# Optimization experiments

Hardware: AMD Instinct MI355X
Metric: run time of the kernel (lower is better)

## Reference

```python
import jax, jax.numpy as jnp
import numpy as np

B, N, C_IN, C_OUT, K = 8, 2048, 64, 128, 20
EPS = 1e-5  # BatchNorm2d default eps


def setup_inputs() -> dict:
    key = jax.random.key(0)
    k1, k2 = jax.random.split(key, 2)
    x = jax.random.normal(k1, (B, C_IN, N), dtype=jnp.float32)
    fan_in = 2 * C_IN
    W = jax.random.normal(k2, (C_OUT, 2 * C_IN), dtype=jnp.float32) / np.sqrt(fan_in).astype(np.float32)
    b = jnp.zeros((C_OUT,), jnp.float32)
    gamma = jnp.ones((C_OUT,), jnp.float32)
    beta = jnp.zeros((C_OUT,), jnp.float32)
    return {"x": x, "W": W, "b": b, "gamma": gamma, "beta": beta}


def reference(x, W, b, gamma, beta):
    # x: (B, C_in, N) -> points (B, N, C_in)
    pts = jnp.transpose(x, (0, 2, 1))
    # pairwise squared L2 distances (B, N, N)
    sq = jnp.sum(pts * pts, axis=-1)
    dist = sq[:, :, None] + sq[:, None, :] - 2.0 * jnp.einsum('bnc,bmc->bnm', pts, pts)
    # knn: top-k of negated distance -> k nearest neighbors (includes self)
    _, nn_idx = jax.lax.top_k(-dist, K)  # (B, N, K)
    # gather neighbor features per batch: (B, N, K, C_in)
    neigh = jax.vmap(lambda p, i: p[i])(pts, nn_idx)
    central = pts[:, :, None, :]  # (B, N, 1, C_in)
    edge = jnp.concatenate(
        [jnp.broadcast_to(central, neigh.shape), neigh - central], axis=-1
    )  # (B, N, K, 2*C_in)
    # 1x1 conv == channelwise linear: (B, N, K, C_out)
    y = jnp.einsum('bnkc,oc->bnko', edge, W) + b
    # BatchNorm2d (training mode): stats over batch + spatial dims, biased var
    mean = jnp.mean(y, axis=(0, 1, 2))
    var = jnp.var(y, axis=(0, 1, 2))
    y = (y - mean) * jax.lax.rsqrt(var + EPS) * gamma + beta
    y = jax.nn.relu(y)
    y = jnp.max(y, axis=2)  # max over k neighbors -> (B, N, C_out)
    return jnp.transpose(y, (0, 2, 1))[..., None]  # (B, C_out, N, 1)
```

## Files before the change

### kernel.cpp

```cpp
#include <hip/hip_runtime.h>
#include <cstdint>
#include <cstddef>

#define NPTS 2048
#define BATCH 8
#define CIN 64
#define CO 128
#define KNN 20
#define KSEL 24
#define NSPLIT 4
#define MKP 25

typedef short s16x8 __attribute__((ext_vector_type(8)));
typedef unsigned short u16x8 __attribute__((ext_vector_type(8)));
typedef float f32x4 __attribute__((ext_vector_type(4)));

__device__ inline unsigned short f2bf_rne(float x) {
  unsigned u = __float_as_uint(x);
  unsigned r = (u + 0x7FFFu + ((u >> 16) & 1u)) >> 16;
  return (unsigned short)r;
}
__device__ inline float bf2f(unsigned short h) {
  return __uint_as_float(((unsigned)h) << 16);
}
__device__ inline unsigned med3u(unsigned a, unsigned b, unsigned c) {
  unsigned d;
  asm("v_med3_u32 %0, %1, %2, %3" : "=v"(d) : "v"(a), "v"(b), "v"(c));
  return d;
}

__global__ __launch_bounds__(256) void prep_kernel(
    const float* __restrict__ x, float* __restrict__ P,
    unsigned short* __restrict__ PG, float* __restrict__ SQ,
    float* __restrict__ STATS) {
  __shared__ float tile[64 * 65];
  const int b = blockIdx.y, T = blockIdx.x, n0 = T * 64, tid = threadIdx.x;
  if (b == 0 && T == 0) {
    for (int t = tid; t < 5 * CO; t += 256) STATS[t] = 0.f;
  }
  const float* xb = x + (size_t)b * CIN * NPTS;
#pragma unroll
  for (int j = 0; j < 16; ++j) {
    int e = j * 256 + tid;
    int c = e >> 6, nl = e & 63;
    tile[c * 65 + nl] = xb[(size_t)c * NPTS + n0 + nl];
  }
  __syncthreads();
  float* Pb = P + (size_t)b * NPTS * CIN;
#pragma unroll
  for (int j = 0; j < 16; ++j) {
    int e = j * 256 + tid;
    int nl = e >> 6, c = e & 63;
    Pb[(size_t)(n0 + nl) * CIN + c] = tile[c * 65 + nl];
  }
  if (tid < 64) {
    float acc = 0.f;
#pragma unroll
    for (int c = 0; c < 64; ++c) {
      float v = tile[c * 65 + tid];
      acc = fmaf(v, v, acc);
    }
    SQ[(size_t)b * NPTS + n0 + tid] = acc;
  }
  const size_t tbase = (size_t)(b * 32 + T) * 8192;
#pragma unroll
  for (int j = 0; j < 2; ++j) {
    int c2 = j * 256 + tid;
    int row = c2 >> 3, kc = c2 & 7;
    int frag = ((row >> 4) << 1) | (kc >> 2);
    int lidx = (row & 15) | ((kc & 3) << 4);
    s16x8 hi8, lo8;
#pragma unroll
    for (int e = 0; e < 8; ++e) {
      float v = tile[(kc * 8 + e) * 65 + row];
      unsigned short hb = f2bf_rne(v);
      float hf = bf2f(hb);
      unsigned short lb = f2bf_rne(v - hf);
      hi8[e] = (short)hb;
      lo8[e] = (short)lb;
    }
    size_t co = (size_t)(frag * 64 + lidx) * 8;
    *(s16x8*)(PG + tbase + co) = hi8;
    *(s16x8*)(PG + tbase + 4096 + co) = lo8;
  }
}

__global__ __launch_bounds__(256) void knn_part_kernel(
    const unsigned short* __restrict__ PG, const float* __restrict__ SQ,
    unsigned* __restrict__ POOLS) {
  const int b = blockIdx.z;
  const int cs = blockIdx.y;
  const int n0 = blockIdx.x * 64;
  const int tid = threadIdx.x;
  const int lane = tid & 63, w = tid >> 6;
  const int qi = w * 16 + (lane & 15);
  const int sub = lane >> 4;
  const int T0 = cs * 8;

  __shared__ unsigned mk[64 * 4 * MKP];

  const size_t tqb = (size_t)(b * 32 + (n0 >> 6)) * 8192;
  const s16x8 qhi0 = *(const s16x8*)(PG + tqb + (size_t)((w * 2 + 0) * 64 + lane) * 8);
  const s16x8 qhi1 = *(const s16x8*)(PG + tqb + (size_t)((w * 2 + 1) * 64 + lane) * 8);
  const s16x8 qlo0 = *(const s16x8*)(PG + tqb + 4096 + (size_t)((w * 2 + 0) * 64 + lane) * 8);
  const s16x8 qlo1 = *(const s16x8*)(PG + tqb + 4096 + (size_t)((w * 2 + 1) * 64 + lane) * 8);

  unsigned hk[KSEL];
#pragma unroll
  for (int s = 0; s < KSEL; ++s) hk[s] = 0xFFFFFFFFu;

#pragma unroll 1
  for (int t = 0; t < 8; ++t) {
    const int T = T0 + t;
    const unsigned short* tb = PG + (size_t)(b * 32 + T) * 8192;
#pragma unroll
    for (int rt = 0; rt < 4; ++rt) {
      const s16x8 ahi0 = *(const s16x8*)(tb + (size_t)((rt * 2 + 0) * 64 + lane) * 8);
      const s16x8 ahi1 = *(const s16x8*)(tb + (size_t)((rt * 2 + 1) * 64 + lane) * 8);
      const s16x8 alo0 = *(const s16x8*)(tb + 4096 + (size_t)((rt * 2 + 0) * 64 + lane) * 8);
      const s16x8 alo1 = *(const s16x8*)(tb + 4096 + (size_t)((rt * 2 + 1) * 64 + lane) * 8);
      f32x4 acc = {0.f, 0.f, 0.f, 0.f};
      acc = __builtin_amdgcn_mfma_f32_16x16x32_bf16(alo0, qhi0, acc, 0, 0, 0);
      acc = __builtin_amdgcn_mfma_f32_16x16x32_bf16(ahi0, qlo0, acc, 0, 0, 0);
      acc = __builtin_amdgcn_mfma_f32_16x16x32_bf16(ahi0, qhi0, acc, 0, 0, 0);
      acc = __builtin_amdgcn_mfma_f32_16x16x32_bf16(alo1, qhi1, acc, 0, 0, 0);
      acc = __builtin_amdgcn_mfma_f32_16x16x32_bf16(ahi1, qlo1, acc, 0, 0, 0);
      acc = __builtin_amdgcn_mfma_f32_16x16x32_bf16(ahi1, qhi1, acc, 0, 0, 0);
      const float4 sq4 = *(const float4*)(SQ + b * NPTS + T * 64 + rt * 16 + sub * 4);
      const float sqa[4] = {sq4.x, sq4.y, sq4.z, sq4.w};
      const int mbase = T * 64 + rt * 16 + sub * 4;
#pragma unroll
      for (int r = 0; r < 4; ++r) {
        float d = fmaf(acc[r], -2.0f, sqa[r]);
        unsigned u = __float_as_uint(d);
        unsigned ord = u ^ (unsigned)(((int)u >> 31) | 0x80000000);
        unsigned key = (ord & 0xFFFFF800u) | (unsigned)(mbase + r);
#pragma unroll
        for (int s = KSEL - 1; s >= 1; --s) hk[s] = med3u(hk[s - 1], hk[s], key);
        hk[0] = hk[0] < key ? hk[0] : key;
      }
    }
  }

#pragma unroll
  for (int s = 0; s < KSEL; ++s) mk[(qi * 4 + sub) * MKP + s] = hk[s];
  __syncthreads();

  if (sub == 0) {
    const unsigned* bl = mk + qi * 4 * MKP;
    unsigned* pq = POOLS + ((size_t)(b * NPTS + n0 + qi) * NSPLIT + cs) * KSEL;
    int p0 = 0, p1 = 0, p2 = 0, p3 = 0;
#pragma unroll 1
    for (int s = 0; s < KSEL; ++s) {
      unsigned k0 = (p0 < KSEL) ? bl[0 * MKP + p0] : 0xFFFFFFFFu;
      unsigned k1 = (p1 < KSEL) ? bl[1 * MKP + p1] : 0xFFFFFFFFu;
      unsigned k2 = (p2 < KSEL) ? bl[2 * MKP + p2] : 0xFFFFFFFFu;
      unsigned k3 = (p3 < KSEL) ? bl[3 * MKP + p3] : 0xFFFFFFFFu;
      unsigned bk = k0; int bs = 0;
      if (k1 < bk) { bk = k1; bs = 1; }
      if (k2 < bk) { bk = k2; bs = 2; }
      if (k3 < bk) { bk = k3; bs = 3; }
      pq[s] = bk;
      if (bs == 0) ++p0; else if (bs == 1) ++p1; else if (bs == 2) ++p2; else ++p3;
    }
  }
}

__global__ __launch_bounds__(256) void knn_merge_kernel(
    const float* __restrict__ P, const unsigned* __restrict__ POOLS,
    int* __restrict__ IDX) {
  const int tid = threadIdx.x;
  const int qi = tid >> 3, st = tid & 7;
  const int r0 = blockIdx.x * 32;
  const int r = r0 + qi;
  const int b = r >> 11;

  __shared__ unsigned lists[32][NSPLIT][KSEL];
  __shared__ unsigned pool[32][KSEL];
  __shared__ double cd[32][KSEL];

  {
    const unsigned* src = POOLS + (size_t)r0 * NSPLIT * KSEL;
    for (int t = tid; t < 32 * NSPLIT * KSEL; t += 256) ((unsigned*)lists)[t] = src[t];
  }
  __syncthreads();

  if (st == 0) {
    const unsigned* bl = &lists[qi][0][0];
    unsigned* pq = &pool[qi][0];
    int p0 = 0, p1 = 0, p2 = 0, p3 = 0;
#pragma unroll 1
    for (int s = 0; s < KSEL; ++s) {
      unsigned k0 = (p0 < KSEL) ? bl[0 * KSEL + p0] : 0xFFFFFFFFu;
      unsigned k1 = (p1 < KSEL) ? bl[1 * KSEL + p1] : 0xFFFFFFFFu;
      unsigned k2 = (p2 < KSEL) ? bl[2 * KSEL + p2] : 0xFFFFFFFFu;
      unsigned k3 = (p3 < KSEL) ? bl[3 * KSEL + p3] : 0xFFFFFFFFu;
      unsigned bk = k0; int bs = 0;
      if (k1 < bk) { bk = k1; bs = 1; }
      if (k2 < bk) { bk = k2; bs = 2; }
      if (k3 < bk) { bk = k3; bs = 3; }
      pq[s] = bk;
      if (bs == 0) ++p0; else if (bs == 1) ++p1; else if (bs == 2) ++p2; else ++p3;
    }
  }
  __syncthreads();

  const float* qrow = P + ((size_t)r << 6);
  float4 q4[16];
#pragma unroll
  for (int t = 0; t < 16; ++t) q4[t] = ((const float4*)qrow)[t];
#pragma unroll 1
  for (int j = 0; j < 3; ++j) {
    int cand = st * 3 + j;
    unsigned key = pool[qi][cand];
    int m = (int)(key & 0x7FFu);
    const float* prow = P + ((size_t)(b * NPTS + m) << 6);
    double a0 = 0.0, a1 = 0.0;
#pragma unroll
    for (int t = 0; t < 16; ++t) {
      float4 pv = ((const float4*)prow)[t];
      double d0 = (double)pv.x - (double)q4[t].x;
      double d1 = (double)pv.y - (double)q4[t].y;
      double d2 = (double)pv.z - (double)q4[t].z;
      double d3 = (double)pv.w - (double)q4[t].w;
      a0 = fma(d1, d1, fma(d0, d0, a0));
      a1 = fma(d3, d3, fma(d2, d2, a1));
    }
    cd[qi][cand] = a0 + a1;
  }
  __syncthreads();

  int* op = IDX + (size_t)r * KNN;
#pragma unroll 1
  for (int j = 0; j < 3; ++j) {
    int cand = st * 3 + j;
    double dv = cd[qi][cand];
    int iv = (int)(pool[qi][cand] & 0x7FFu);
    int rk = 0;
#pragma unroll 1
    for (int t = 0; t < KSEL; ++t) {
      double dt = cd[qi][t];
      int it = (int)(pool[qi][t] & 0x7FFu);
      rk += ((dt < dv) || (dt == dv && it < iv)) ? 1 : 0;
    }
    if (rk < KNN) op[rk] = iv;
  }
}

__global__ __launch_bounds__(256) void proj_kernel(
    const float* __restrict__ P, const float* __restrict__ W,
    float* __restrict__ U, unsigned short* __restrict__ Vh) {
  const int r0 = blockIdx.x * 64;
  const int o0 = blockIdx.y * 32;
  const int tid = threadIdx.x;
  const int og = tid & 3;
  const int nl = tid >> 2;

  __shared__ float Pt[64 * 65];
  __shared__ float Wu_s[64 * 36];
  __shared__ float Wd_s[64 * 36];

#pragma unroll
  for (int j = 0; j < 16; ++j) {
    int e = j * 256 + tid;
    int c = e & 63, rl = e >> 6;
    Pt[rl * 65 + c] = P[((size_t)(r0 + rl) << 6) + c];
  }
#pragma unroll
  for (int j = 0; j < 8; ++j) {
    int e = j * 256 + tid;
    int c = e & 63, ol = e >> 6;
    float w1 = W[(size_t)(o0 + ol) * 128 + c];
    float w2 = W[(size_t)(o0 + ol) * 128 + 64 + c];
    Wu_s[c * 36 + ol] = w1 - w2;
    Wd_s[c * 36 + ol] = w2;
  }
  __syncthreads();

  float au[8] = {0,0,0,0,0,0,0,0};
  float av[8] = {0,0,0,0,0,0,0,0};
#pragma unroll 4
  for (int c = 0; c < 64; ++c) {
    float p = Pt[nl * 65 + c];
    const float* wu = Wu_s + c * 36 + og * 8;
    const float* wd = Wd_s + c * 36 + og * 8;
    float4 u0 = *(const float4*)wu;
    float4 u1 = *(const float4*)(wu + 4);
    float4 dd0 = *(const float4*)wd;
    float4 dd1 = *(const float4*)(wd + 4);
    au[0] = fmaf(p, u0.x, au[0]); au[1] = fmaf(p, u0.y, au[1]);
    au[2] = fmaf(p, u0.z, au[2]); au[3] = fmaf(p, u0.w, au[3]);
    au[4] = fmaf(p, u1.x, au[4]); au[5] = fmaf(p, u1.y, au[5]);
    au[6] = fmaf(p, u1.z, au[6]); au[7] = fmaf(p, u1.w, au[7]);
    av[0] = fmaf(p, dd0.x, av[0]); av[1] = fmaf(p, dd0.y, av[1]);
    av[2] = fmaf(p, dd0.z, av[2]); av[3] = fmaf(p, dd0.w, av[3]);
    av[4] = fmaf(p, dd1.x, av[4]); av[5] = fmaf(p, dd1.y, av[5]);
    av[6] = fmaf(p, dd1.z, av[6]); av[7] = fmaf(p, dd1.w, av[7]);
  }
  size_t ob = (size_t)(r0 + nl) * CO + o0 + og * 8;
  float4 s0 = {au[0], au[1], au[2], au[3]};
  float4 s1 = {au[4], au[5], au[6], au[7]};
  *(float4*)(U + ob) = s0;
  *(float4*)(U + ob + 4) = s1;
  u16x8 hv;
#pragma unroll
  for (int j = 0; j < 8; ++j) hv[j] = f2bf_rne(av[j]);
  *(u16x8*)(Vh + ob) = hv;
}

__global__ __launch_bounds__(256) void gstats_kernel(
    const float* __restrict__ U, const unsigned short* __restrict__ Vh,
    const int* __restrict__ IDX, float* __restrict__ Z, float* __restrict__ STATS) {
  const int r0 = blockIdx.x * 16;
  const int tid = threadIdx.x;
  const int og = tid & 15, nl = tid >> 4;
  const int r = r0 + nl;
  const int b = r >> 11;
  const unsigned short* Vb = Vh + ((size_t)b << 11) * CO;

  __shared__ int ii[16 * KNN];
  __shared__ float red[4][5][128];

  for (int t = tid; t < 16 * KNN; t += 256) ii[t] = IDX[(size_t)r0 * KNN + t];
  __syncthreads();

  float vmax[8], svr[8], svvr[8];
#pragma unroll
  for (int j = 0; j < 8; ++j) { vmax[j] = -3.4e38f; svr[j] = 0.f; svvr[j] = 0.f; }
#pragma unroll 1
  for (int k = 0; k < KNN; ++k) {
    int idx = ii[nl * KNN + k];
    u16x8 hv = *(const u16x8*)(Vb + (size_t)idx * CO + og * 8);
#pragma unroll
    for (int j = 0; j < 8; ++j) {
      float v = bf2f((unsigned short)hv[j]);
      vmax[j] = fmaxf(vmax[j], v);
      svr[j] += v;
      svvr[j] = fmaf(v, v, svvr[j]);
    }
  }
  size_t ob = (size_t)r * CO + og * 8;
  float4 u0 = *(const float4*)(U + ob);
  float4 u1 = *(const float4*)(U + ob + 4);
  float uu[8] = {u0.x, u0.y, u0.z, u0.w, u1.x, u1.y, u1.z, u1.w};
  float4 z0 = {uu[0] + vmax[0], uu[1] + vmax[1], uu[2] + vmax[2], uu[3] + vmax[3]};
  float4 z1 = {uu[4] + vmax[4], uu[5] + vmax[5], uu[6] + vmax[6], uu[7] + vmax[7]};
  *(float4*)(Z + ob) = z0;
  *(float4*)(Z + ob + 4) = z1;

  float pu[8], puu[8], psv[8], pusv[8], psvv[8];
#pragma unroll
  for (int j = 0; j < 8; ++j) {
    pu[j] = uu[j];
    puu[j] = uu[j] * uu[j];
    psv[j] = svr[j];
    pusv[j] = uu[j] * svr[j];
    psvv[j] = svvr[j];
  }
#pragma unroll
  for (int j = 0; j < 8; ++j) {
    pu[j]   += __shfl_xor(pu[j], 16);   pu[j]   += __shfl_xor(pu[j], 32);
    puu[j]  += __shfl_xor(puu[j], 16);  puu[j]  += __shfl_xor(puu[j], 32);
    psv[j]  += __shfl_xor(psv[j], 16);  psv[j]  += __shfl_xor(psv[j], 32);
    pusv[j] += __shfl_xor(pusv[j], 16); pusv[j] += __shfl_xor(pusv[j], 32);
    psvv[j] += __shfl_xor(psvv[j], 16); psvv[j] += __shfl_xor(psvv[j], 32);
  }
  const int w = tid >> 6;
  if ((tid & 0x30) == 0) {
#pragma unroll
    for (int j = 0; j < 8; ++j) {
      int c = og * 8 + j;
      red[w][0][c] = pu[j];  red[w][1][c] = puu[j];  red[w][2][c] = psv[j];
      red[w][3][c] = pusv[j]; red[w][4][c] = psvv[j];
    }
  }
  __syncthreads();
  if (tid < 128) {
#pragma unroll
    for (int s = 0; s < 5; ++s) {
      float v4 = red[0][s][tid] + red[1][s][tid] + red[2][s][tid] + red[3][s][tid];
      atomicAdd(&STATS[s * CO + tid], v4);
    }
  }
}

__global__ __launch_bounds__(256) void out_kernel(
    const float* __restrict__ Z, const float* __restrict__ STATS,
    const float* __restrict__ bias, const float* __restrict__ gamma,
    const float* __restrict__ beta, float* __restrict__ out) {
  const int n0 = blockIdx.x * 64, o0 = blockIdx.y * 32, b = blockIdx.z;
  const int tid = threadIdx.x;
  __shared__ float tile[64 * 33];
  __shared__ float fs[32], ft[32];
  if (tid < 32) {
    const int o = o0 + tid;
    const float M = (float)(BATCH * NPTS * KNN);
    const float Kf = (float)KNN;
    float su = STATS[0 * CO + o], suu = STATS[1 * CO + o], ssv = STATS[2 * CO + o];
    float susv = STATS[3 * CO + o], ssvv = STATS[4 * CO + o];
    float bo = bias[o];
    float lin = (Kf * su + ssv) / M;
    float mean = lin + bo;
    float ey2 = (Kf * suu + ssvv + 2.0f * susv) / M + 2.0f * bo * lin + bo * bo;
    float var = ey2 - mean * mean;
    float scale = gamma[o] * rsqrtf(var + 1e-5f);
    fs[tid] = scale;
    ft[tid] = (bo - mean) * scale + beta[o];
  }
#pragma unroll
  for (int j = 0; j < 8; ++j) {
    int e = j * 256 + tid;
    int ol = e & 31, nl = e >> 5;
    tile[nl * 33 + ol] = Z[(size_t)(b * NPTS + n0 + nl) * CO + o0 + ol];
  }
  __syncthreads();
#pragma unroll
  for (int j = 0; j < 8; ++j) {
    int e = j * 256 + tid;
    int nl = e & 63, ol = e >> 6;
    float v = fmaf(tile[nl * 33 + ol], fs[ol], ft[ol]);
    out[(size_t)(b * CO + o0 + ol) * NPTS + n0 + nl] = fmaxf(v, 0.0f);
  }
}

extern "C" void kernel_launch(void* const* d_in, const int* in_sizes, int n_in,
                              void* d_out, int out_size, void* d_ws, size_t ws_size,
                              hipStream_t stream) {
  const float* x = (const float*)d_in[0];
  const float* W = (const float*)d_in[1];
  const float* bias = (const float*)d_in[2];
  const float* gamma = (const float*)d_in[3];
  const float* beta = (const float*)d_in[4];
  float* out = (float*)d_out;
  float* ws = (float*)d_ws;

  const size_t NR = (size_t)BATCH * NPTS;
  size_t off = 0;
  float* P = ws + off;                      off += NR * CIN;
  unsigned short* PG = (unsigned short*)(ws + off); off += NR * CIN;
  float* SQ = ws + off;                     off += NR;
  int* IDX = (int*)(ws + off);              off += NR * KNN;
  float* U = ws + off;                      off += NR * CO;
  unsigned short* Vh = (unsigned short*)(ws + off); off += NR * CO / 2;
  float* STATS = ws + off;                  off += 5 * CO;
  unsigned* POOLS = (unsigned*)U;
  float* Z = ws;
  if (ws_size < off * sizeof(float)) return;

  prep_kernel<<<dim3(NPTS / 64, BATCH), 256, 0, stream>>>(x, P, PG, SQ, STATS);
  knn_part_kernel<<<dim3(NPTS / 64, NSPLIT, BATCH), 256, 0, stream>>>(PG, SQ, POOLS);
  knn_merge_kernel<<<dim3(NR / 32), 256, 0, stream>>>(P, POOLS, IDX);
  proj_kernel<<<dim3(NR / 64, CO / 32), 256, 0, stream>>>(P, W, U, Vh);
  gstats_kernel<<<dim3(NR / 16), 256, 0, stream>>>(U, Vh, IDX, Z, STATS);
  out_kernel<<<dim3(NPTS / 64, CO / 32, BATCH), 256, 0, stream>>>(Z, STATS, bias, gamma, beta, out);
}
```

Baseline: 146.1 us.

## Merge knn partial and projection kernels into one interleaved launch

Combines the kNN partial top-k kernel and the projection GEMM into a single 2048-block launch. Even blocks do kNN work and odd blocks do the projection, so the independent projection overlaps with the compute-heavy kNN and one launch is removed. POOLS moves from aliasing U into its own workspace region, because U is now written concurrently. Shared memory becomes a union sized for the larger branch, which may lower occupancy for the kNN blocks.

After: 168.9 us. 15.6% more time.

```diff
diff --git a/kernel.cpp b/kernel.cpp
--- a/kernel.cpp
+++ b/kernel.cpp
@@ -85,84 +85,148 @@
   }
 }
 
-__global__ __launch_bounds__(256) void knn_part_kernel(
+__global__ __launch_bounds__(256) void knn_proj_kernel(
     const unsigned short* __restrict__ PG, const float* __restrict__ SQ,
-    unsigned* __restrict__ POOLS) {
-  const int b = blockIdx.z;
-  const int cs = blockIdx.y;
-  const int n0 = blockIdx.x * 64;
+    unsigned* __restrict__ POOLS, const float* __restrict__ P,
+    const float* __restrict__ W, float* __restrict__ U,
+    unsigned short* __restrict__ Vh) {
+  __shared__ __align__(16) char smem[35072];
   const int tid = threadIdx.x;
-  const int lane = tid & 63, w = tid >> 6;
-  const int qi = w * 16 + (lane & 15);
-  const int sub = lane >> 4;
-  const int T0 = cs * 8;
-
-  __shared__ unsigned mk[64 * 4 * MKP];
-
-  const size_t tqb = (size_t)(b * 32 + (n0 >> 6)) * 8192;
-  const s16x8 qhi0 = *(const s16x8*)(PG + tqb + (size_t)((w * 2 + 0) * 64 + lane) * 8);
-  const s16x8 qhi1 = *(const s16x8*)(PG + tqb + (size_t)((w * 2 + 1) * 64 + lane) * 8);
-  const s16x8 qlo0 = *(const s16x8*)(PG + tqb + 4096 + (size_t)((w * 2 + 0) * 64 + lane) * 8);
-  const s16x8 qlo1 = *(const s16x8*)(PG + tqb + 4096 + (size_t)((w * 2 + 1) * 64 + lane) * 8);
-
-  unsigned hk[KSEL];
-#pragma unroll
-  for (int s = 0; s < KSEL; ++s) hk[s] = 0xFFFFFFFFu;
-
-#pragma unroll 1
-  for (int t = 0; t < 8; ++t) {
-    const int T = T0 + t;
-    const unsigned short* tb = PG + (size_t)(b * 32 + T) * 8192;
-#pragma unroll
-    for (int rt = 0; rt < 4; ++rt) {
-      const s16x8 ahi0 = *(const s16x8*)(tb + (size_t)((rt * 2 + 0) * 64 + lane) * 8);
-      const s16x8 ahi1 = *(const s16x8*)(tb + (size_t)((rt * 2 + 1) * 64 + lane) * 8);
-      const s16x8 alo0 = *(const s16x8*)(tb + 4096 + (size_t)((rt * 2 + 0) * 64 + lane) * 8);
-      const s16x8 alo1 = *(const s16x8*)(tb + 4096 + (size_t)((rt * 2 + 1) * 64 + lane) * 8);
-      f32x4 acc = {0.f, 0.f, 0.f, 0.f};
-      acc = __builtin_amdgcn_mfma_f32_16x16x32_bf16(alo0, qhi0, acc, 0, 0, 0);
-      acc = __builtin_amdgcn_mfma_f32_16x16x32_bf16(ahi0, qlo0, acc, 0, 0, 0);
-      acc = __builtin_amdgcn_mfma_f32_16x16x32_bf16(ahi0, qhi0, acc, 0, 0, 0);
-      acc = __builtin_amdgcn_mfma_f32_16x16x32_bf16(alo1, qhi1, acc, 0, 0, 0);
-      acc = __builtin_amdgcn_mfma_f32_16x16x32_bf16(ahi1, qlo1, acc, 0, 0, 0);
-      acc = __builtin_amdgcn_mfma_f32_16x16x32_bf16(ahi1, qhi1, acc, 0, 0, 0);
-      const float4 sq4 = *(const float4*)(SQ + b * NPTS + T * 64 + rt * 16 + sub * 4);
-      const float sqa[4] = {sq4.x, sq4.y, sq4.z, sq4.w};
-      const int mbase = T * 64 + rt * 16 + sub * 4;
-#pragma unroll
-      for (int r = 0; r < 4; ++r) {
-        float d = fmaf(acc[r], -2.0f, sqa[r]);
-        unsigned u = __float_as_uint(d);
-        unsigned ord = u ^ (unsigned)(((int)u >> 31) | 0x80000000);
-        unsigned key = (ord & 0xFFFFF800u) | (unsigned)(mbase + r);
-#pragma unroll
-        for (int s = KSEL - 1; s >= 1; --s) hk[s] = med3u(hk[s - 1], hk[s], key);
-        hk[0] = hk[0] < key ? hk[0] : key;
+
+  if ((blockIdx.x & 1) == 0) {
+    const int kblk = blockIdx.x >> 1;
+    const int qt = kblk & 31;
+    const int cs = (kblk >> 5) & 3;
+    const int b = kblk >> 7;
+    const int n0 = qt * 64;
+    const int lane = tid & 63, w = tid >> 6;
+    const int qi = w * 16 + (lane & 15);
+    const int sub = lane >> 4;
+    const int T0 = cs * 8;
+
+    unsigned* mk = (unsigned*)smem;
+
+    const size_t tqb = (size_t)(b * 32 + qt) * 8192;
+    const s16x8 qhi0 = *(const s16x8*)(PG + tqb + (size_t)((w * 2 + 0) * 64 + lane) * 8);
+    const s16x8 qhi1 = *(const s16x8*)(PG + tqb + (size_t)((w * 2 + 1) * 64 + lane) * 8);
+    const s16x8 qlo0 = *(const s16x8*)(PG + tqb + 4096 + (size_t)((w * 2 + 0) * 64 + lane) * 8);
+    const s16x8 qlo1 = *(const s16x8*)(PG + tqb + 4096 + (size_t)((w * 2 + 1) * 64 + lane) * 8);
+
+    unsigned hk[KSEL];
+#pragma unroll
+    for (int s = 0; s < KSEL; ++s) hk[s] = 0xFFFFFFFFu;
+
+#pragma unroll 1
+    for (int t = 0; t < 8; ++t) {
+      const int T = T0 + t;
+      const unsigned short* tb = PG + (size_t)(b * 32 + T) * 8192;
+#pragma unroll
+      for (int rt = 0; rt < 4; ++rt) {
+        const s16x8 ahi0 = *(const s16x8*)(tb + (size_t)((rt * 2 + 0) * 64 + lane) * 8);
+        const s16x8 ahi1 = *(const s16x8*)(tb + (size_t)((rt * 2 + 1) * 64 + lane) * 8);
+        const s16x8 alo0 = *(const s16x8*)(tb + 4096 + (size_t)((rt * 2 + 0) * 64 + lane) * 8);
+        const s16x8 alo1 = *(const s16x8*)(tb + 4096 + (size_t)((rt * 2 + 1) * 64 + lane) * 8);
+        f32x4 acc = {0.f, 0.f, 0.f, 0.f};
+        acc = __builtin_amdgcn_mfma_f32_16x16x32_bf16(alo0, qhi0, acc, 0, 0, 0);
+        acc = __builtin_amdgcn_mfma_f32_16x16x32_bf16(ahi0, qlo0, acc, 0, 0, 0);
+        acc = __builtin_amdgcn_mfma_f32_16x16x32_bf16(ahi0, qhi0, acc, 0, 0, 0);
+        acc = __builtin_amdgcn_mfma_f32_16x16x32_bf16(alo1, qhi1, acc, 0, 0, 0);
+        acc = __builtin_amdgcn_mfma_f32_16x16x32_bf16(ahi1, qlo1, acc, 0, 0, 0);
+        acc = __builtin_amdgcn_mfma_f32_16x16x32_bf16(ahi1, qhi1, acc, 0, 0, 0);
+        const float4 sq4 = *(const float4*)(SQ + b * NPTS + T * 64 + rt * 16 + sub * 4);
+        const float sqa[4] = {sq4.x, sq4.y, sq4.z, sq4.w};
+        const int mbase = T * 64 + rt * 16 + sub * 4;
+#pragma unroll
+        for (int r = 0; r < 4; ++r) {
+          float d = fmaf(acc[r], -2.0f, sqa[r]);
+          unsigned u = __float_as_uint(d);
+          unsigned ord = u ^ (unsigned)(((int)u >> 31) | 0x80000000);
+          unsigned key = (ord & 0xFFFFF800u) | (unsigned)(mbase + r);
+#pragma unroll
+          for (int s = KSEL - 1; s >= 1; --s) hk[s] = med3u(hk[s - 1], hk[s], key);
+          hk[0] = hk[0] < key ? hk[0] : key;
+        }
       }
     }
-  }
-
-#pragma unroll
-  for (int s = 0; s < KSEL; ++s) mk[(qi * 4 + sub) * MKP + s] = hk[s];
-  __syncthreads();
-
-  if (sub == 0) {
-    const unsigned* bl = mk + qi * 4 * MKP;
-    unsigned* pq = POOLS + ((size_t)(b * NPTS + n0 + qi) * NSPLIT + cs) * KSEL;
-    int p0 = 0, p1 = 0, p2 = 0, p3 = 0;
-#pragma unroll 1
-    for (int s = 0; s < KSEL; ++s) {
-      unsigned k0 = (p0 < KSEL) ? bl[0 * MKP + p0] : 0xFFFFFFFFu;
-      unsigned k1 = (p1 < KSEL) ? bl[1 * MKP + p1] : 0xFFFFFFFFu;
-      unsigned k2 = (p2 < KSEL) ? bl[2 * MKP + p2] : 0xFFFFFFFFu;
-      unsigned k3 = (p3 < KSEL) ? bl[3 * MKP + p3] : 0xFFFFFFFFu;
-      unsigned bk = k0; int bs = 0;
-      if (k1 < bk) { bk = k1; bs = 1; }
-      if (k2 < bk) { bk = k2; bs = 2; }
-      if (k3 < bk) { bk = k3; bs = 3; }
-      pq[s] = bk;
-      if (bs == 0) ++p0; else if (bs == 1) ++p1; else if (bs == 2) ++p2; else ++p3;
-    }
+
+#pragma unroll
+    for (int s = 0; s < KSEL; ++s) mk[(qi * 4 + sub) * MKP + s] = hk[s];
+    __syncthreads();
+
+    if (sub == 0) {
+      const unsigned* bl = mk + qi * 4 * MKP;
+      unsigned* pq = POOLS + ((size_t)(b * NPTS + n0 + qi) * NSPLIT + cs) * KSEL;
+      int p0 = 0, p1 = 0, p2 = 0, p3 = 0;
+#pragma unroll 1
+      for (int s = 0; s < KSEL; ++s) {
+        unsigned k0 = (p0 < KSEL) ? bl[0 * MKP + p0] : 0xFFFFFFFFu;
+        unsigned k1 = (p1 < KSEL) ? bl[1 * MKP + p1] : 0xFFFFFFFFu;
+        unsigned k2 = (p2 < KSEL) ? bl[2 * MKP + p2] : 0xFFFFFFFFu;
+        unsigned k3 = (p3 < KSEL) ? bl[3 * MKP + p3] : 0xFFFFFFFFu;
+        unsigned bk = k0; int bs = 0;
+        if (k1 < bk) { bk = k1; bs = 1; }
+        if (k2 < bk) { bk = k2; bs = 2; }
+        if (k3 < bk) { bk = k3; bs = 3; }
+        pq[s] = bk;
+        if (bs == 0) ++p0; else if (bs == 1) ++p1; else if (bs == 2) ++p2; else ++p3;
+      }
+    }
+  } else {
+    const int pblk = blockIdx.x >> 1;
+    const int r0 = (pblk >> 2) * 64;
+    const int o0 = (pblk & 3) * 32;
+    const int og = tid & 3;
+    const int nl = tid >> 2;
+    float* Pt = (float*)smem;
+    float* Wu_s = Pt + 64 * 65;
+    float* Wd_s = Wu_s + 64 * 36;
+
+#pragma unroll
+    for (int j = 0; j < 16; ++j) {
+      int e = j * 256 + tid;
+      int c = e & 63, rl = e >> 6;
+      Pt[rl * 65 + c] = P[((size_t)(r0 + rl) << 6) + c];
+    }
+#pragma unroll
+    for (int j = 0; j < 8; ++j) {
+      int e = j * 256 + tid;
+      int c = e & 63, ol = e >> 6;
+      float w1 = W[(size_t)(o0 + ol) * 128 + c];
+      float w2 = W[(size_t)(o0 + ol) * 128 + 64 + c];
+      Wu_s[c * 36 + ol] = w1 - w2;
+      Wd_s[c * 36 + ol] = w2;
+    }
+    __syncthreads();
+
+    float au[8] = {0,0,0,0,0,0,0,0};
+    float av[8] = {0,0,0,0,0,0,0,0};
+#pragma unroll 4
+    for (int c = 0; c < 64; ++c) {
+      float p = Pt[nl * 65 + c];
+      const float* wu = Wu_s + c * 36 + og * 8;
+      const float* wd = Wd_s + c * 36 + og * 8;
+      float4 u0 = *(const float4*)wu;
+      float4 u1 = *(const float4*)(wu + 4);
+      float4 dd0 = *(const float4*)wd;
+      float4 dd1 = *(const float4*)(wd + 4);
+      au[0] = fmaf(p, u0.x, au[0]); au[1] = fmaf(p, u0.y, au[1]);
+      au[2] = fmaf(p, u0.z, au[2]); au[3] = fmaf(p, u0.w, au[3]);
+      au[4] = fmaf(p, u1.x, au[4]); au[5] = fmaf(p, u1.y, au[5]);
+      au[6] = fmaf(p, u1.z, au[6]); au[7] = fmaf(p, u1.w, au[7]);
+      av[0] = fmaf(p, dd0.x, av[0]); av[1] = fmaf(p, dd0.y, av[1]);
+      av[2] = fmaf(p, dd0.z, av[2]); av[3] = fmaf(p, dd0.w, av[3]);
+      av[4] = fmaf(p, dd1.x, av[4]); av[5] = fmaf(p, dd1.y, av[5]);
+      av[6] = fmaf(p, dd1.z, av[6]); av[7] = fmaf(p, dd1.w, av[7]);
+    }
+    size_t ob = (size_t)(r0 + nl) * CO + o0 + og * 8;
+    float4 s0 = {au[0], au[1], au[2], au[3]};
+    float4 s1 = {au[4], au[5], au[6], au[7]};
+    *(float4*)(U + ob) = s0;
+    *(float4*)(U + ob + 4) = s1;
+    u16x8 hv;
+#pragma unroll
+    for (int j = 0; j < 8; ++j) hv[j] = f2bf_rne(av[j]);
+    *(u16x8*)(Vh + ob) = hv;
   }
 }
 
@@ -245,67 +309,6 @@
     }
     if (rk < KNN) op[rk] = iv;
   }
-}
-
-__global__ __launch_bounds__(256) void proj_kernel(
-    const float* __restrict__ P, const float* __restrict__ W,
-    float* __restrict__ U, unsigned short* __restrict__ Vh) {
-  const int r0 = blockIdx.x * 64;
-  const int o0 = blockIdx.y * 32;
-  const int tid = threadIdx.x;
-  const int og = tid & 3;
-  const int nl = tid >> 2;
-
-  __shared__ float Pt[64 * 65];
-  __shared__ float Wu_s[64 * 36];
-  __shared__ float Wd_s[64 * 36];
-
-#pragma unroll
-  for (int j = 0; j < 16; ++j) {
-    int e = j * 256 + tid;
-    int c = e & 63, rl = e >> 6;
-    Pt[rl * 65 + c] = P[((size_t)(r0 + rl) << 6) + c];
-  }
-#pragma unroll
-  for (int j = 0; j < 8; ++j) {
-    int e = j * 256 + tid;
-    int c = e & 63, ol = e >> 6;
-    float w1 = W[(size_t)(o0 + ol) * 128 + c];
-    float w2 = W[(size_t)(o0 + ol) * 128 + 64 + c];
-    Wu_s[c * 36 + ol] = w1 - w2;
-    Wd_s[c * 36 + ol] = w2;
-  }
-  __syncthreads();
-
-  float au[8] = {0,0,0,0,0,0,0,0};
-  float av[8] = {0,0,0,0,0,0,0,0};
-#pragma unroll 4
-  for (int c = 0; c < 64; ++c) {
-    float p = Pt[nl * 65 + c];
-    const float* wu = Wu_s + c * 36 + og * 8;
-    const float* wd = Wd_s + c * 36 + og * 8;
-    float4 u0 = *(const float4*)wu;
-    float4 u1 = *(const float4*)(wu + 4);
-    float4 dd0 = *(const float4*)wd;
-    float4 dd1 = *(const float4*)(wd + 4);
-    au[0] = fmaf(p, u0.x, au[0]); au[1] = fmaf(p, u0.y, au[1]);
-    au[2] = fmaf(p, u0.z, au[2]); au[3] = fmaf(p, u0.w, au[3]);
-    au[4] = fmaf(p, u1.x, au[4]); au[5] = fmaf(p, u1.y, au[5]);
-    au[6] = fmaf(p, u1.z, au[6]); au[7] = fmaf(p, u1.w, au[7]);
-    av[0] = fmaf(p, dd0.x, av[0]); av[1] = fmaf(p, dd0.y, av[1]);
-    av[2] = fmaf(p, dd0.z, av[2]); av[3] = fmaf(p, dd0.w, av[3]);
-    av[4] = fmaf(p, dd1.x, av[4]); av[5] = fmaf(p, dd1.y, av[5]);
-    av[6] = fmaf(p, dd1.z, av[6]); av[7] = fmaf(p, dd1.w, av[7]);
-  }
-  size_t ob = (size_t)(r0 + nl) * CO + o0 + og * 8;
-  float4 s0 = {au[0], au[1], au[2], au[3]};
-  float4 s1 = {au[4], au[5], au[6], au[7]};
-  *(float4*)(U + ob) = s0;
-  *(float4*)(U + ob + 4) = s1;
-  u16x8 hv;
-#pragma unroll
-  for (int j = 0; j < 8; ++j) hv[j] = f2bf_rne(av[j]);
-  *(u16x8*)(Vh + ob) = hv;
 }
 
 __global__ __launch_bounds__(256) void gstats_kernel(
@@ -442,15 +445,14 @@
   int* IDX = (int*)(ws + off);              off += NR * KNN;
   float* U = ws + off;                      off += NR * CO;
   unsigned short* Vh = (unsigned short*)(ws + off); off += NR * CO / 2;
+  unsigned* POOLS = (unsigned*)(ws + off);  off += NR * NSPLIT * KSEL;
   float* STATS = ws + off;                  off += 5 * CO;
-  unsigned* POOLS = (unsigned*)U;
   float* Z = ws;
   if (ws_size < off * sizeof(float)) return;
 
   prep_kernel<<<dim3(NPTS / 64, BATCH), 256, 0, stream>>>(x, P, PG, SQ, STATS);
-  knn_part_kernel<<<dim3(NPTS / 64, NSPLIT, BATCH), 256, 0, stream>>>(PG, SQ, POOLS);
+  knn_proj_kernel<<<dim3(2048), 256, 0, stream>>>(PG, SQ, POOLS, P, W, U, Vh);
   knn_merge_kernel<<<dim3(NR / 32), 256, 0, stream>>>(P, POOLS, IDX);
-  proj_kernel<<<dim3(NR / 64, CO / 32), 256, 0, stream>>>(P, W, U, Vh);
   gstats_kernel<<<dim3(NR / 16), 256, 0, stream>>>(U, Vh, IDX, Z, STATS);
   out_kernel<<<dim3(NPTS / 64, CO / 32, BATCH), 256, 0, stream>>>(Z, STATS, bias, gamma, beta, out);
 }
```
